# Kernel optimization log

Hardware: AMD Instinct MI355X
Metric: run time of the kernel (lower is better)

The kernel has to match this reference:

```python
import jax, jax.numpy as jnp
import numpy as np

R, N, E, F, D, A = 3, 50000, 800000, 128, 128, 64
EPS = 1e-5


def setup_inputs() -> dict:
    key = jax.random.key(0)
    ks = jax.random.split(key, 8)
    s = 0.05
    feat = jax.random.normal(ks[0], (N, F), jnp.float32)
    src = jax.random.randint(ks[1], (R, E), 0, N)
    dst = jax.random.randint(ks[2], (R, E), 0, N)
    W0 = jax.random.normal(ks[3], (R, F, D), jnp.float32) * s
    b0 = jnp.zeros((R, D), jnp.float32)
    W1 = jax.random.normal(ks[4], (R, D, D), jnp.float32) * s
    b1 = jnp.zeros((R, D), jnp.float32)
    ln_g = jnp.ones((R, D), jnp.float32)   # per-relation MessageTransform LayerNorm (shared across its 2 layers)
    ln_b = jnp.zeros((R, D), jnp.float32)
    LN_g = jnp.ones((D,), jnp.float32)     # final PROVGEM layer_norm
    LN_b = jnp.zeros((D,), jnp.float32)
    Wa1 = jax.random.normal(ks[5], (R, D, A), jnp.float32) * s  # semantic attention proj
    Wa2 = jax.random.normal(ks[6], (R, A), jnp.float32) * s     # semantic attention score vec
    return dict(feat=feat, src=src, dst=dst, W0=W0, b0=b0, W1=W1, b1=b1,
                ln_g=ln_g, ln_b=ln_b, LN_g=LN_g, LN_b=LN_b, Wa1=Wa1, Wa2=Wa2)


def _ln(x, g, b):
    mu = jnp.mean(x, axis=-1, keepdims=True)
    var = jnp.mean(jnp.square(x - mu), axis=-1, keepdims=True)
    return (x - mu) * jax.lax.rsqrt(var + EPS) * g + b


def _mean_agg(feat, src_r, dst_r):
    # copy_u + mean: gather source feats along edges, segment-mean into dst nodes
    msg = feat[src_r]                                            # [E, F]
    ssum = jax.ops.segment_sum(msg, dst_r, num_segments=N)       # [N, F]
    deg = jax.ops.segment_sum(jnp.ones((E,), feat.dtype), dst_r, num_segments=N)
    return ssum / jnp.maximum(deg, 1.0)[:, None]                 # 0 for zero-degree nodes


def reference(feat, src, dst, W0, b0, W1, b1, ln_g, ln_b, LN_g, LN_b, Wa1, Wa2):
    # per-relation aggregation (loop over small fixed R=3)
    neigh = jnp.stack([_mean_agg(feat, src[r], dst[r]) for r in range(R)])  # [R, N, F]
    h = feat[None, :, :] + neigh                                            # residual add
    x = jnp.einsum('rnf,rfd->rnd', h, W0) + b0[:, None, :]
    x = jax.nn.relu(_ln(x, ln_g[:, None, :], ln_b[:, None, :]))
    x = jnp.einsum('rnd,rde->rne', x, W1) + b1[:, None, :]
    x = jax.nn.relu(_ln(x, ln_g[:, None, :], ln_b[:, None, :]))
    # final LayerNorm over [R, N, D]
    h = _ln(x, LN_g, LN_b)
    # semantic attention over relations
    e = jnp.einsum('rna,ra->rn', jnp.tanh(jnp.einsum('rnd,rda->rna', h, Wa1)), Wa2)
    attn = jax.nn.softmax(e, axis=0)                                        # softmax over relations
    return jnp.einsum('rn,rnd->nd', attn, h)                                # [N, D]
```

## Files before the change

kernel.cpp:

```cpp
#include <hip/hip_runtime.h>

#define RR 3
#define NN 50000
#define EE 800000
#define FF 128
#define DD 128
#define AA 64
#define EPSF 1e-5f
#define RN (RR * NN)
#define RE (RR * EE)
#define NTPR ((NN + 127) / 128)
#define NBK (RR * NTPR)
#define ECHUNK 8192
#define NEBLK ((RE + ECHUNK - 1) / ECHUNK)
#define NTILES (NN / 16)

typedef __attribute__((ext_vector_type(8))) short bf16x8;
typedef __attribute__((ext_vector_type(4))) float f32x4;

__device__ __forceinline__ short f2bs(float x) {
    union { float f; unsigned u; } v; v.f = x;
    unsigned rr = (v.u + 0x7fffu + ((v.u >> 16) & 1u)) >> 16;
    return (short)(rr & 0xffffu);
}

__device__ __forceinline__ float bs2f_lo(int p) {
    union { unsigned u; float f; } v; v.u = (unsigned)p << 16; return v.f;
}
__device__ __forceinline__ float bs2f_hi(int p) {
    union { unsigned u; float f; } v; v.u = (unsigned)p & 0xffff0000u; return v.f;
}

__device__ __forceinline__ int rel_of(long e) {
    return (e >= 2L * EE) ? 2 : ((e >= (long)EE) ? 1 : 0);
}

__device__ __forceinline__ float ftanh(float x) {
    float a = __expf(2.0f * fabsf(x));
    return copysignf(1.0f - 2.0f / (a + 1.0f), x);
}

__global__ __launch_bounds__(256)
void feat2bf16(const float* __restrict__ feat, short* __restrict__ featb) {
    int gid = blockIdx.x * blockDim.x + threadIdx.x;
    if (gid >= NN * 16) return;
    f32x4 a = ((const f32x4*)feat)[2 * gid];
    f32x4 b = ((const f32x4*)feat)[2 * gid + 1];
    bf16x8 o;
    o[0] = f2bs(a.x); o[1] = f2bs(a.y); o[2] = f2bs(a.z); o[3] = f2bs(a.w);
    o[4] = f2bs(b.x); o[5] = f2bs(b.y); o[6] = f2bs(b.z); o[7] = f2bs(b.w);
    ((bf16x8*)featb)[gid] = o;
}

__global__ __launch_bounds__(256)
void count_kernel(const int* __restrict__ dst, int* __restrict__ bcnt) {
    __shared__ int hist[NBK];
    for (int i = threadIdx.x; i < NBK; i += 256) hist[i] = 0;
    __syncthreads();
    long ebase = (long)blockIdx.x * ECHUNK;
    for (int i = threadIdx.x; i < ECHUNK; i += 256) {
        long e = ebase + i;
        if (e < RE)
            atomicAdd(&hist[rel_of(e) * NTPR + (dst[e] >> 7)], 1);
    }
    __syncthreads();
    for (int i = threadIdx.x; i < NBK; i += 256) {
        int v = hist[i];
        if (v) atomicAdd(&bcnt[i], v);
    }
}

__global__ __launch_bounds__(256)
void bscan_kernel(const int* __restrict__ bcnt, int* __restrict__ bstart,
                  int* __restrict__ boff) {
    __shared__ int sm[256];
    int t = threadIdx.x;
    int loc[5];
    int s = 0;
    #pragma unroll
    for (int i = 0; i < 5; ++i) {
        int idx = t * 5 + i;
        int v = (idx < NBK) ? bcnt[idx] : 0;
        loc[i] = v; s += v;
    }
    sm[t] = s;
    __syncthreads();
    for (int d = 1; d < 256; d <<= 1) {
        int u = (t >= d) ? sm[t - d] : 0;
        __syncthreads();
        sm[t] += u;
        __syncthreads();
    }
    int run = sm[t] - s;
    #pragma unroll
    for (int i = 0; i < 5; ++i) {
        int idx = t * 5 + i;
        if (idx < NBK) { bstart[idx] = run; boff[idx] = run; run += loc[i]; }
    }
}

__global__ __launch_bounds__(256)
void bscatterA(const int* __restrict__ src, const int* __restrict__ dst,
               int* __restrict__ boff, unsigned* __restrict__ bpair) {
    __shared__ int hist[NBK];
    __shared__ int base[NBK];
    for (int i = threadIdx.x; i < NBK; i += 256) hist[i] = 0;
    __syncthreads();
    long ebase = (long)blockIdx.x * ECHUNK;
    for (int i = threadIdx.x; i < ECHUNK; i += 256) {
        long e = ebase + i;
        if (e < RE)
            atomicAdd(&hist[rel_of(e) * NTPR + (dst[e] >> 7)], 1);
    }
    __syncthreads();
    for (int i = threadIdx.x; i < NBK; i += 256) {
        int v = hist[i];
        base[i] = v ? atomicAdd(&boff[i], v) : 0;
    }
    __syncthreads();
    for (int i = threadIdx.x; i < ECHUNK; i += 256) {
        long e = ebase + i;
        if (e < RE) {
            int r = rel_of(e);
            int d = dst[e];
            int b = r * NTPR + (d >> 7);
            int pos = atomicAdd(&base[b], 1);
            bpair[pos] = ((unsigned)(d & 127) << 16) | (unsigned)src[e];
        }
    }
}

__global__ __launch_bounds__(256)
void scatterB(const unsigned* __restrict__ bpair, const int* __restrict__ bstart,
              const int* __restrict__ bcnt,
              int* __restrict__ off, int* __restrict__ cnt,
              int* __restrict__ csr) {
    __shared__ int hist[128];
    __shared__ int pre[128];
    __shared__ int base[128];
    int b = blockIdx.x;
    int r = b / NTPR, tile = b - r * NTPR;
    const int t = threadIdx.x;
    if (t < 128) hist[t] = 0;
    __syncthreads();
    int start = bstart[b], end = start + bcnt[b];
    for (int i = start + t; i < end; i += 256)
        atomicAdd(&hist[bpair[i] >> 16], 1);
    __syncthreads();
    if (t < 128) pre[t] = hist[t];
    __syncthreads();
    for (int d = 1; d < 128; d <<= 1) {
        int v = (t < 128 && t >= d) ? pre[t - d] : 0;
        __syncthreads();
        if (t < 128) pre[t] += v;
        __syncthreads();
    }
    if (t < 128) {
        int excl = pre[t] - hist[t];
        base[t] = start + excl;
        int nloc = tile * 128 + t;
        if (nloc < NN) {
            off[r * NN + nloc] = start + excl;
            cnt[r * NN + nloc] = hist[t];
        }
        hist[t] = 0;
    }
    __syncthreads();
    for (int i = start + t; i < end; i += 256) {
        unsigned p = bpair[i];
        int d = (int)(p >> 16);
        int rank = atomicAdd(&hist[d], 1);
        csr[base[d] + rank] = (int)(p & 0xFFFFu);
    }
}

__global__ __launch_bounds__(256)
void gather_kernel(const short* __restrict__ featb,
                   const int* __restrict__ csr,
                   const int* __restrict__ off,
                   const int* __restrict__ cnt,
                   short* __restrict__ ssumb) {
    int gid = blockIdx.x * blockDim.x + threadIdx.x;
    int w = gid >> 6, lane = gid & 63;
    if (w >= RN) return;
    int c = cnt[w];
    int start = off[w];
    int end = start + c;
    const int* f2 = (const int*)featb;
    float ax0 = 0.f, ay0 = 0.f, ax1 = 0.f, ay1 = 0.f;
    float ax2 = 0.f, ay2 = 0.f, ax3 = 0.f, ay3 = 0.f;
    float ax4 = 0.f, ay4 = 0.f, ax5 = 0.f, ay5 = 0.f;
    float ax6 = 0.f, ay6 = 0.f, ax7 = 0.f, ay7 = 0.f;
    int j = start;
    for (; j + 7 < end; j += 8) {
        int s0 = csr[j + 0], s1 = csr[j + 1], s2 = csr[j + 2], s3 = csr[j + 3];
        int s4 = csr[j + 4], s5 = csr[j + 5], s6 = csr[j + 6], s7 = csr[j + 7];
        int v0 = f2[(size_t)s0 * 64 + lane];
        int v1 = f2[(size_t)s1 * 64 + lane];
        int v2 = f2[(size_t)s2 * 64 + lane];
        int v3 = f2[(size_t)s3 * 64 + lane];
        int v4 = f2[(size_t)s4 * 64 + lane];
        int v5 = f2[(size_t)s5 * 64 + lane];
        int v6 = f2[(size_t)s6 * 64 + lane];
        int v7 = f2[(size_t)s7 * 64 + lane];
        ax0 += bs2f_lo(v0); ay0 += bs2f_hi(v0);
        ax1 += bs2f_lo(v1); ay1 += bs2f_hi(v1);
        ax2 += bs2f_lo(v2); ay2 += bs2f_hi(v2);
        ax3 += bs2f_lo(v3); ay3 += bs2f_hi(v3);
        ax4 += bs2f_lo(v4); ay4 += bs2f_hi(v4);
        ax5 += bs2f_lo(v5); ay5 += bs2f_hi(v5);
        ax6 += bs2f_lo(v6); ay6 += bs2f_hi(v6);
        ax7 += bs2f_lo(v7); ay7 += bs2f_hi(v7);
    }
    for (; j + 3 < end; j += 4) {
        int s0 = csr[j + 0], s1 = csr[j + 1], s2 = csr[j + 2], s3 = csr[j + 3];
        int v0 = f2[(size_t)s0 * 64 + lane];
        int v1 = f2[(size_t)s1 * 64 + lane];
        int v2 = f2[(size_t)s2 * 64 + lane];
        int v3 = f2[(size_t)s3 * 64 + lane];
        ax0 += bs2f_lo(v0); ay0 += bs2f_hi(v0);
        ax1 += bs2f_lo(v1); ay1 += bs2f_hi(v1);
        ax2 += bs2f_lo(v2); ay2 += bs2f_hi(v2);
        ax3 += bs2f_lo(v3); ay3 += bs2f_hi(v3);
    }
    for (; j < end; ++j) {
        int s = csr[j];
        int v = f2[(size_t)s * 64 + lane];
        ax0 += bs2f_lo(v); ay0 += bs2f_hi(v);
    }
    float ax = ((ax0 + ax1) + (ax2 + ax3)) + ((ax4 + ax5) + (ax6 + ax7));
    float ay = ((ay0 + ay1) + (ay2 + ay3)) + ((ay4 + ay5) + (ay6 + ay7));
    float inv = 1.0f / fmaxf((float)c, 1.0f);
    int n = w % NN;
    int fv = f2[(size_t)n * 64 + lane];
    float hx = bs2f_lo(fv) + ax * inv;
    float hy = bs2f_hi(fv) + ay * inv;
    unsigned plo = (unsigned short)f2bs(hx);
    unsigned phi = (unsigned short)f2bs(hy);
    ((int*)ssumb)[(size_t)w * 64 + lane] = (int)((phi << 16) | plo);
}


__device__ __forceinline__ void mfma_layer(const bf16x8 A[4], const short* Wlds,
                                           int g8, int c, f32x4 acc[8]) {
    #pragma unroll
    for (int kk = 0; kk < 4; ++kk) {
        #pragma unroll
        for (int t = 0; t < 8; ++t) {
            int d = t * 16 + c;
            bf16x8 B = *(const bf16x8*)&Wlds[d * 128 + ((kk * 32 + g8) ^ ((d & 7) << 3))];
            acc[t] = __builtin_amdgcn_mfma_f32_16x16x32_bf16(A[kk], B, acc[t], 0, 0, 0);
        }
    }
}

template <bool RELU, bool BIAS>
__device__ __forceinline__ void ln_block(f32x4 acc[8], const float* bias,
                                         const float* gam, const float* bet, int c) {
    float s0 = 0, s1 = 0, s2 = 0, s3 = 0, p0 = 0, p1 = 0, p2 = 0, p3 = 0;
    #pragma unroll
    for (int t = 0; t < 8; ++t) {
        if (BIAS) {
            float bb = bias[t * 16 + c];
            acc[t][0] += bb; acc[t][1] += bb;
            acc[t][2] += bb; acc[t][3] += bb;
        }
        s0 += acc[t][0]; p0 += acc[t][0] * acc[t][0];
        s1 += acc[t][1]; p1 += acc[t][1] * acc[t][1];
        s2 += acc[t][2]; p2 += acc[t][2] * acc[t][2];
        s3 += acc[t][3]; p3 += acc[t][3] * acc[t][3];
    }
    #pragma unroll
    for (int m = 1; m < 16; m <<= 1) {
        s0 += __shfl_xor(s0, m); s1 += __shfl_xor(s1, m);
        s2 += __shfl_xor(s2, m); s3 += __shfl_xor(s3, m);
        p0 += __shfl_xor(p0, m); p1 += __shfl_xor(p1, m);
        p2 += __shfl_xor(p2, m); p3 += __shfl_xor(p3, m);
    }
    const float inv = 1.0f / 128.0f;
    float mu0 = s0 * inv, mu1 = s1 * inv, mu2 = s2 * inv, mu3 = s3 * inv;
    float r0 = rsqrtf(p0 * inv - mu0 * mu0 + EPSF);
    float r1 = rsqrtf(p1 * inv - mu1 * mu1 + EPSF);
    float r2 = rsqrtf(p2 * inv - mu2 * mu2 + EPSF);
    float r3 = rsqrtf(p3 * inv - mu3 * mu3 + EPSF);
    #pragma unroll
    for (int t = 0; t < 8; ++t) {
        float gg = gam[t * 16 + c], bb = bet[t * 16 + c];
        float v0 = (acc[t][0] - mu0) * r0 * gg + bb;
        float v1 = (acc[t][1] - mu1) * r1 * gg + bb;
        float v2 = (acc[t][2] - mu2) * r2 * gg + bb;
        float v3 = (acc[t][3] - mu3) * r3 * gg + bb;
        if (RELU) {
            v0 = fmaxf(v0, 0.f); v1 = fmaxf(v1, 0.f);
            v2 = fmaxf(v2, 0.f); v3 = fmaxf(v3, 0.f);
        }
        acc[t][0] = v0; acc[t][1] = v1;
        acc[t][2] = v2; acc[t][3] = v3;
    }
}

__device__ __forceinline__ void store_ht(const f32x4 acc[8], short* myht, int g, int c) {
    #pragma unroll
    for (int t = 0; t < 8; ++t) {
        int col = t * 16 + c;
        #pragma unroll
        for (int qq = 0; qq < 4; ++qq) {
            int row = g * 4 + qq;
            myht[row * 128 + (col ^ ((row & 7) << 3))] = f2bs(acc[t][qq]);
        }
    }
}

__device__ __forceinline__ void ht_to_global(const short* myht, short* gout, int g, int c) {
    #pragma unroll
    for (int cc = 0; cc < 4; ++cc) {
        int row = cc * 4 + g;
        int col0 = c * 8;
        bf16x8 v = *(const bf16x8*)&myht[row * 128 + (col0 ^ ((row & 7) << 3))];
        *(bf16x8*)&gout[row * FF + col0] = v;
    }
}

__global__ __launch_bounds__(512)
void fused_l1(short* hbuf,
              const float* __restrict__ W0, const float* __restrict__ b0,
              const float* __restrict__ ln_g, const float* __restrict__ ln_b) {
    __shared__ short W0t[FF * DD];
    __shared__ short ht[8][16 * DD];
    __shared__ float b0s[DD], lgs[DD], lbs[DD];

    const int r = blockIdx.y;
    const int tid = threadIdx.x;

    for (int i = tid; i < FF * DD; i += 512) {
        int k = i >> 7, d = i & 127;
        W0t[d * 128 + (k ^ ((d & 7) << 3))] = f2bs(W0[(size_t)r * FF * DD + i]);
    }
    if (tid < DD) {
        b0s[tid] = b0[r * DD + tid];
        lgs[tid] = ln_g[r * DD + tid];
        lbs[tid] = ln_b[r * DD + tid];
    }
    __syncthreads();

    const int wv = tid >> 6, ln = tid & 63;
    const int g = ln >> 4, c = ln & 15;
    const int g8 = g * 8;
    short* myht = ht[wv];

    for (int tile = blockIdx.x * 8 + wv; tile < NTILES; tile += gridDim.x * 8) {
        const int nbase = tile * 16;
        bf16x8 A[4];
        {
            const short* sp = hbuf + ((size_t)r * NN + nbase + c) * FF;
            #pragma unroll
            for (int kk = 0; kk < 4; ++kk)
                A[kk] = *(const bf16x8*)(sp + kk * 32 + g8);
        }
        f32x4 acc[8];
        #pragma unroll
        for (int t = 0; t < 8; ++t) acc[t] = (f32x4){0.f, 0.f, 0.f, 0.f};
        mfma_layer(A, W0t, g8, c, acc);
        ln_block<true, true>(acc, b0s, lgs, lbs, c);
        store_ht(acc, myht, g, c);
        ht_to_global(myht, hbuf + ((size_t)r * NN + nbase) * FF, g, c);
    }
}

__global__ __launch_bounds__(512)
void fused_l2(short* hbuf,
              const float* __restrict__ W1, const float* __restrict__ b1,
              const float* __restrict__ ln_g, const float* __restrict__ ln_b,
              const float* __restrict__ LN_g, const float* __restrict__ LN_b) {
    __shared__ short W1t[DD * DD];
    __shared__ short ht[8][16 * DD];
    __shared__ float b1s[DD], lgs[DD], lbs[DD], Lgs[DD], Lbs[DD];

    const int r = blockIdx.y;
    const int tid = threadIdx.x;

    for (int i = tid; i < DD * DD; i += 512) {
        int k = i >> 7, d = i & 127;
        W1t[d * 128 + (k ^ ((d & 7) << 3))] = f2bs(W1[(size_t)r * DD * DD + i]);
    }
    if (tid < DD) {
        b1s[tid] = b1[r * DD + tid];
        lgs[tid] = ln_g[r * DD + tid];
        lbs[tid] = ln_b[r * DD + tid];
        Lgs[tid] = LN_g[tid];
        Lbs[tid] = LN_b[tid];
    }
    __syncthreads();

    const int wv = tid >> 6, ln = tid & 63;
    const int g = ln >> 4, c = ln & 15;
    const int g8 = g * 8;
    short* myht = ht[wv];

    for (int tile = blockIdx.x * 8 + wv; tile < NTILES; tile += gridDim.x * 8) {
        const int nbase = tile * 16;
        bf16x8 A[4];
        {
            const short* sp = hbuf + ((size_t)r * NN + nbase + c) * FF;
            #pragma unroll
            for (int kk = 0; kk < 4; ++kk)
                A[kk] = *(const bf16x8*)(sp + kk * 32 + g8);
        }
        f32x4 acc[8];
        #pragma unroll
        for (int t = 0; t < 8; ++t) acc[t] = (f32x4){0.f, 0.f, 0.f, 0.f};
        mfma_layer(A, W1t, g8, c, acc);
        ln_block<true, true>(acc, b1s, lgs, lbs, c);
        ln_block<false, false>(acc, nullptr, Lgs, Lbs, c);
        store_ht(acc, myht, g, c);
        ht_to_global(myht, hbuf + ((size_t)r * NN + nbase) * FF, g, c);
    }
}

__global__ __launch_bounds__(256)
void attn_score(const short* __restrict__ hbuf,
                const float* __restrict__ Wa1, const float* __restrict__ Wa2,
                float* __restrict__ evec) {
    __shared__ short Wa1t[RR][AA * DD];
    __shared__ float wa2s[RR][AA];

    const int tid = threadIdx.x;
    for (int i = tid; i < RR * DD * AA; i += 256) {
        int r2 = i >> 13;
        int rem = i & 8191;
        int k = rem >> 6, a = rem & 63;
        Wa1t[r2][a * 128 + (k ^ ((a & 7) << 3))] = f2bs(Wa1[i]);
    }
    if (tid < RR * AA) wa2s[tid >> 6][tid & 63] = Wa2[tid];
    __syncthreads();

    const int wv = tid >> 6, ln = tid & 63;
    const int col = ln & 15, g = ln >> 4;
    const int g8 = g * 8, g4 = g * 4;

    for (int idx = blockIdx.x * 4 + wv; idx < RR * NTILES; idx += gridDim.x * 4) {
        int r = idx / NTILES;
        int tile = idx - r * NTILES;
        int nbase = tile * 16;
        const short* hrow = hbuf + ((size_t)r * NN + nbase + col) * FF;

        f32x4 acc[4];
        #pragma unroll
        for (int t = 0; t < 4; ++t) acc[t] = (f32x4){0.f, 0.f, 0.f, 0.f};
        #pragma unroll
        for (int kk = 0; kk < 4; ++kk) {
            bf16x8 Bh = *(const bf16x8*)(hrow + kk * 32 + g8);
            #pragma unroll
            for (int t = 0; t < 4; ++t) {
                int a_ = t * 16 + col;
                bf16x8 Wf = *(const bf16x8*)&Wa1t[r][a_ * 128 + ((kk * 32 + g8) ^ ((a_ & 7) << 3))];
                acc[t] = __builtin_amdgcn_mfma_f32_16x16x32_bf16(Wf, Bh, acc[t], 0, 0, 0);
            }
        }
        float e = 0.f;
        #pragma unroll
        for (int t = 0; t < 4; ++t) {
            f32x4 wv2 = *(const f32x4*)&wa2s[r][t * 16 + g4];
            e += ftanh(acc[t][0]) * wv2[0] + ftanh(acc[t][1]) * wv2[1]
               + ftanh(acc[t][2]) * wv2[2] + ftanh(acc[t][3]) * wv2[3];
        }
        e += __shfl_xor(e, 16);
        e += __shfl_xor(e, 32);
        if (ln < 16) evec[(size_t)r * NN + nbase + ln] = e;
    }
}

__global__ __launch_bounds__(256)
void combine_kernel(const short* __restrict__ hfb,
                    const float* __restrict__ evec,
                    float* __restrict__ out) {
    int gid = blockIdx.x * blockDim.x + threadIdx.x;
    if (gid >= NN * 64) return;
    int n = gid >> 6, j = gid & 63;
    float e0 = evec[n], e1 = evec[NN + n], e2 = evec[2 * NN + n];
    float m = fmaxf(e0, fmaxf(e1, e2));
    float w0 = __expf(e0 - m), w1 = __expf(e1 - m), w2 = __expf(e2 - m);
    float inv = 1.0f / (w0 + w1 + w2);
    w0 *= inv; w1 *= inv; w2 *= inv;
    const int* h0 = (const int*)hfb + (size_t)n * 64;
    const int* h1 = (const int*)hfb + ((size_t)NN + n) * 64;
    const int* h2 = (const int*)hfb + ((size_t)2 * NN + n) * 64;
    int a = h0[j], b = h1[j], d = h2[j];
    float2 o;
    o.x = w0 * bs2f_lo(a) + w1 * bs2f_lo(b) + w2 * bs2f_lo(d);
    o.y = w0 * bs2f_hi(a) + w1 * bs2f_hi(b) + w2 * bs2f_hi(d);
    ((float2*)out)[(size_t)n * 64 + j] = o;
}

extern "C" void kernel_launch(void* const* d_in, const int* in_sizes, int n_in,
                              void* d_out, int out_size, void* d_ws, size_t ws_size,
                              hipStream_t stream) {
    const float* feat = (const float*)d_in[0];
    const int*   src  = (const int*)d_in[1];
    const int*   dst  = (const int*)d_in[2];
    const float* W0   = (const float*)d_in[3];
    const float* b0   = (const float*)d_in[4];
    const float* W1   = (const float*)d_in[5];
    const float* b1   = (const float*)d_in[6];
    const float* ln_g = (const float*)d_in[7];
    const float* ln_b = (const float*)d_in[8];
    const float* LN_g = (const float*)d_in[9];
    const float* LN_b = (const float*)d_in[10];
    const float* Wa1  = (const float*)d_in[11];
    const float* Wa2  = (const float*)d_in[12];
    float* out = (float*)d_out;

    short*    ssumb  = (short*)d_ws;
    short*    featb  = ssumb + (size_t)RN * FF;
    int*      cnt    = (int*)(featb + (size_t)NN * FF);
    int*      off    = cnt + RN;
    int*      csr    = off + RN;
    float*    evec   = (float*)(csr + RE);
    int*      bcnt   = (int*)(evec + RN);
    int*      bstart = bcnt + NBK;
    int*      boff   = bstart + NBK;
    unsigned* bpair  = (unsigned*)(boff + NBK);

    feat2bf16<<<(NN * 16 + 255) / 256, 256, 0, stream>>>(feat, featb);
    hipMemsetAsync(bcnt, 0, (size_t)NBK * sizeof(int), stream);
    count_kernel<<<NEBLK, 256, 0, stream>>>(dst, bcnt);
    bscan_kernel<<<1, 256, 0, stream>>>(bcnt, bstart, boff);
    bscatterA<<<NEBLK, 256, 0, stream>>>(src, dst, boff, bpair);
    scatterB<<<NBK, 256, 0, stream>>>(bpair, bstart, bcnt, off, cnt, csr);
    gather_kernel<<<(RN * 64 + 255) / 256, 256, 0, stream>>>(featb, csr, off, cnt, ssumb);

    const int GX = (NTILES + 7) / 8;
    fused_l1<<<dim3(GX, RR), 512, 0, stream>>>(ssumb, W0, b0, ln_g, ln_b);
    fused_l2<<<dim3(GX, RR), 512, 0, stream>>>(ssumb, W1, b1, ln_g, ln_b, LN_g, LN_b);
    attn_score<<<512, 256, 0, stream>>>(ssumb, Wa1, Wa2, evec);
    combine_kernel<<<(NN * 64 + 255) / 256, 256, 0, stream>>>(ssumb, evec, out);
}
```

Before: 312.4 us.

## Gather neighbor features in fp8 and fuse attention scoring with combine

```diff
diff --git a/kernel.cpp b/kernel.cpp
--- a/kernel.cpp
+++ b/kernel.cpp
@@ -17,6 +17,7 @@
 
 typedef __attribute__((ext_vector_type(8))) short bf16x8;
 typedef __attribute__((ext_vector_type(4))) float f32x4;
+typedef __attribute__((ext_vector_type(2))) float f32x2;
 
 __device__ __forceinline__ short f2bs(float x) {
     union { float f; unsigned u; } v; v.f = x;
@@ -41,7 +42,8 @@
 }
 
 __global__ __launch_bounds__(256)
-void feat2bf16(const float* __restrict__ feat, short* __restrict__ featb) {
+void feat2both(const float* __restrict__ feat, short* __restrict__ featb,
+               int* __restrict__ featq) {
     int gid = blockIdx.x * blockDim.x + threadIdx.x;
     if (gid >= NN * 16) return;
     f32x4 a = ((const f32x4*)feat)[2 * gid];
@@ -50,6 +52,13 @@
     o[0] = f2bs(a.x); o[1] = f2bs(a.y); o[2] = f2bs(a.z); o[3] = f2bs(a.w);
     o[4] = f2bs(b.x); o[5] = f2bs(b.y); o[6] = f2bs(b.z); o[7] = f2bs(b.w);
     ((bf16x8*)featb)[gid] = o;
+    int lo = 0, hi = 0;
+    lo = __builtin_amdgcn_cvt_pk_fp8_f32(a.x, a.y, lo, false);
+    lo = __builtin_amdgcn_cvt_pk_fp8_f32(a.z, a.w, lo, true);
+    hi = __builtin_amdgcn_cvt_pk_fp8_f32(b.x, b.y, hi, false);
+    hi = __builtin_amdgcn_cvt_pk_fp8_f32(b.z, b.w, hi, true);
+    int2 pk; pk.x = lo; pk.y = hi;
+    ((int2*)featq)[gid] = pk;
 }
 
 __global__ __launch_bounds__(256)
@@ -176,6 +185,7 @@
 
 __global__ __launch_bounds__(256)
 void gather_kernel(const short* __restrict__ featb,
+                   const int* __restrict__ featq,
                    const int* __restrict__ csr,
                    const int* __restrict__ off,
                    const int* __restrict__ cnt,
@@ -186,7 +196,7 @@
     int c = cnt[w];
     int start = off[w];
     int end = start + c;
-    const int* f2 = (const int*)featb;
+    const unsigned short* q = (const unsigned short*)featq;
     float ax0 = 0.f, ay0 = 0.f, ax1 = 0.f, ay1 = 0.f;
     float ax2 = 0.f, ay2 = 0.f, ax3 = 0.f, ay3 = 0.f;
     float ax4 = 0.f, ay4 = 0.f, ax5 = 0.f, ay5 = 0.f;
@@ -195,44 +205,57 @@
     for (; j + 7 < end; j += 8) {
         int s0 = csr[j + 0], s1 = csr[j + 1], s2 = csr[j + 2], s3 = csr[j + 3];
         int s4 = csr[j + 4], s5 = csr[j + 5], s6 = csr[j + 6], s7 = csr[j + 7];
-        int v0 = f2[(size_t)s0 * 64 + lane];
-        int v1 = f2[(size_t)s1 * 64 + lane];
-        int v2 = f2[(size_t)s2 * 64 + lane];
-        int v3 = f2[(size_t)s3 * 64 + lane];
-        int v4 = f2[(size_t)s4 * 64 + lane];
-        int v5 = f2[(size_t)s5 * 64 + lane];
-        int v6 = f2[(size_t)s6 * 64 + lane];
-        int v7 = f2[(size_t)s7 * 64 + lane];
-        ax0 += bs2f_lo(v0); ay0 += bs2f_hi(v0);
-        ax1 += bs2f_lo(v1); ay1 += bs2f_hi(v1);
-        ax2 += bs2f_lo(v2); ay2 += bs2f_hi(v2);
-        ax3 += bs2f_lo(v3); ay3 += bs2f_hi(v3);
-        ax4 += bs2f_lo(v4); ay4 += bs2f_hi(v4);
-        ax5 += bs2f_lo(v5); ay5 += bs2f_hi(v5);
-        ax6 += bs2f_lo(v6); ay6 += bs2f_hi(v6);
-        ax7 += bs2f_lo(v7); ay7 += bs2f_hi(v7);
+        int v0 = q[(size_t)s0 * 64 + lane];
+        int v1 = q[(size_t)s1 * 64 + lane];
+        int v2 = q[(size_t)s2 * 64 + lane];
+        int v3 = q[(size_t)s3 * 64 + lane];
+        int v4 = q[(size_t)s4 * 64 + lane];
+        int v5 = q[(size_t)s5 * 64 + lane];
+        int v6 = q[(size_t)s6 * 64 + lane];
+        int v7 = q[(size_t)s7 * 64 + lane];
+        f32x2 f0 = __builtin_amdgcn_cvt_pk_f32_fp8(v0, false);
+        f32x2 f1 = __builtin_amdgcn_cvt_pk_f32_fp8(v1, false);
+        f32x2 f2v = __builtin_amdgcn_cvt_pk_f32_fp8(v2, false);
+        f32x2 f3 = __builtin_amdgcn_cvt_pk_f32_fp8(v3, false);
+        f32x2 f4 = __builtin_amdgcn_cvt_pk_f32_fp8(v4, false);
+        f32x2 f5 = __builtin_amdgcn_cvt_pk_f32_fp8(v5, false);
+        f32x2 f6 = __builtin_amdgcn_cvt_pk_f32_fp8(v6, false);
+        f32x2 f7 = __builtin_amdgcn_cvt_pk_f32_fp8(v7, false);
+        ax0 += f0[0]; ay0 += f0[1];
+        ax1 += f1[0]; ay1 += f1[1];
+        ax2 += f2v[0]; ay2 += f2v[1];
+        ax3 += f3[0]; ay3 += f3[1];
+        ax4 += f4[0]; ay4 += f4[1];
+        ax5 += f5[0]; ay5 += f5[1];
+        ax6 += f6[0]; ay6 += f6[1];
+        ax7 += f7[0]; ay7 += f7[1];
     }
     for (; j + 3 < end; j += 4) {
         int s0 = csr[j + 0], s1 = csr[j + 1], s2 = csr[j + 2], s3 = csr[j + 3];
-        int v0 = f2[(size_t)s0 * 64 + lane];
-        int v1 = f2[(size_t)s1 * 64 + lane];
-        int v2 = f2[(size_t)s2 * 64 + lane];
-        int v3 = f2[(size_t)s3 * 64 + lane];
-        ax0 += bs2f_lo(v0); ay0 += bs2f_hi(v0);
-        ax1 += bs2f_lo(v1); ay1 += bs2f_hi(v1);
-        ax2 += bs2f_lo(v2); ay2 += bs2f_hi(v2);
-        ax3 += bs2f_lo(v3); ay3 += bs2f_hi(v3);
+        int v0 = q[(size_t)s0 * 64 + lane];
+        int v1 = q[(size_t)s1 * 64 + lane];
+        int v2 = q[(size_t)s2 * 64 + lane];
+        int v3 = q[(size_t)s3 * 64 + lane];
+        f32x2 f0 = __builtin_amdgcn_cvt_pk_f32_fp8(v0, false);
+        f32x2 f1 = __builtin_amdgcn_cvt_pk_f32_fp8(v1, false);
+        f32x2 f2v = __builtin_amdgcn_cvt_pk_f32_fp8(v2, false);
+        f32x2 f3 = __builtin_amdgcn_cvt_pk_f32_fp8(v3, false);
+        ax0 += f0[0]; ay0 += f0[1];
+        ax1 += f1[0]; ay1 += f1[1];
+        ax2 += f2v[0]; ay2 += f2v[1];
+        ax3 += f3[0]; ay3 += f3[1];
     }
     for (; j < end; ++j) {
         int s = csr[j];
-        int v = f2[(size_t)s * 64 + lane];
-        ax0 += bs2f_lo(v); ay0 += bs2f_hi(v);
+        int v = q[(size_t)s * 64 + lane];
+        f32x2 f0 = __builtin_amdgcn_cvt_pk_f32_fp8(v, false);
+        ax0 += f0[0]; ay0 += f0[1];
     }
     float ax = ((ax0 + ax1) + (ax2 + ax3)) + ((ax4 + ax5) + (ax6 + ax7));
     float ay = ((ay0 + ay1) + (ay2 + ay3)) + ((ay4 + ay5) + (ay6 + ay7));
     float inv = 1.0f / fmaxf((float)c, 1.0f);
     int n = w % NN;
-    int fv = f2[(size_t)n * 64 + lane];
+    int fv = ((const int*)featb)[(size_t)n * 64 + lane];
     float hx = bs2f_lo(fv) + ax * inv;
     float hy = bs2f_hi(fv) + ay * inv;
     unsigned plo = (unsigned short)f2bs(hx);
@@ -418,9 +441,9 @@
 }
 
 __global__ __launch_bounds__(256)
-void attn_score(const short* __restrict__ hbuf,
-                const float* __restrict__ Wa1, const float* __restrict__ Wa2,
-                float* __restrict__ evec) {
+void attn_combine(const short* __restrict__ hbuf,
+                  const float* __restrict__ Wa1, const float* __restrict__ Wa2,
+                  float* __restrict__ out) {
     __shared__ short Wa1t[RR][AA * DD];
     __shared__ float wa2s[RR][AA];
 
@@ -438,58 +461,60 @@
     const int col = ln & 15, g = ln >> 4;
     const int g8 = g * 8, g4 = g * 4;
 
-    for (int idx = blockIdx.x * 4 + wv; idx < RR * NTILES; idx += gridDim.x * 4) {
-        int r = idx / NTILES;
-        int tile = idx - r * NTILES;
-        int nbase = tile * 16;
-        const short* hrow = hbuf + ((size_t)r * NN + nbase + col) * FF;
-
-        f32x4 acc[4];
+    for (int tile = blockIdx.x * 4 + wv; tile < NTILES; tile += gridDim.x * 4) {
+        const int nbase = tile * 16;
+        bf16x8 Bh[RR][4];
+        float e[RR];
         #pragma unroll
-        for (int t = 0; t < 4; ++t) acc[t] = (f32x4){0.f, 0.f, 0.f, 0.f};
+        for (int r = 0; r < RR; ++r) {
+            const short* hrow = hbuf + ((size_t)r * NN + nbase + col) * FF;
+            #pragma unroll
+            for (int kk = 0; kk < 4; ++kk)
+                Bh[r][kk] = *(const bf16x8*)(hrow + kk * 32 + g8);
+            f32x4 acc[4];
+            #pragma unroll
+            for (int t = 0; t < 4; ++t) acc[t] = (f32x4){0.f, 0.f, 0.f, 0.f};
+            #pragma unroll
+            for (int kk = 0; kk < 4; ++kk)
+                #pragma unroll
+                for (int t = 0; t < 4; ++t) {
+                    int a_ = t * 16 + col;
+                    bf16x8 Wf = *(const bf16x8*)&Wa1t[r][a_ * 128 + ((kk * 32 + g8) ^ ((a_ & 7) << 3))];
+                    acc[t] = __builtin_amdgcn_mfma_f32_16x16x32_bf16(Wf, Bh[r][kk], acc[t], 0, 0, 0);
+                }
+            float ee = 0.f;
+            #pragma unroll
+            for (int t = 0; t < 4; ++t) {
+                f32x4 wv2 = *(const f32x4*)&wa2s[r][t * 16 + g4];
+                ee += ftanh(acc[t][0]) * wv2[0] + ftanh(acc[t][1]) * wv2[1]
+                    + ftanh(acc[t][2]) * wv2[2] + ftanh(acc[t][3]) * wv2[3];
+            }
+            ee += __shfl_xor(ee, 16);
+            ee += __shfl_xor(ee, 32);
+            e[r] = ee;
+        }
+        float m = fmaxf(e[0], fmaxf(e[1], e[2]));
+        float w0 = __expf(e[0] - m), w1 = __expf(e[1] - m), w2 = __expf(e[2] - m);
+        float inv = 1.0f / (w0 + w1 + w2);
+        w0 *= inv; w1 *= inv; w2 *= inv;
+
+        float* orow = out + (size_t)(nbase + col) * DD;
         #pragma unroll
         for (int kk = 0; kk < 4; ++kk) {
-            bf16x8 Bh = *(const bf16x8*)(hrow + kk * 32 + g8);
-            #pragma unroll
-            for (int t = 0; t < 4; ++t) {
-                int a_ = t * 16 + col;
-                bf16x8 Wf = *(const bf16x8*)&Wa1t[r][a_ * 128 + ((kk * 32 + g8) ^ ((a_ & 7) << 3))];
-                acc[t] = __builtin_amdgcn_mfma_f32_16x16x32_bf16(Wf, Bh, acc[t], 0, 0, 0);
+            union { bf16x8 v; int i[4]; } u0, u1, u2;
+            u0.v = Bh[0][kk]; u1.v = Bh[1][kk]; u2.v = Bh[2][kk];
+            f32x4 lo, hi;
+            #pragma unroll
+            for (int p = 0; p < 4; ++p) {
+                float va = w0 * bs2f_lo(u0.i[p]) + w1 * bs2f_lo(u1.i[p]) + w2 * bs2f_lo(u2.i[p]);
+                float vb = w0 * bs2f_hi(u0.i[p]) + w1 * bs2f_hi(u1.i[p]) + w2 * bs2f_hi(u2.i[p]);
+                if (p < 2) { lo[2 * p] = va; lo[2 * p + 1] = vb; }
+                else       { hi[2 * (p - 2)] = va; hi[2 * (p - 2) + 1] = vb; }
             }
-        }
-        float e = 0.f;
-        #pragma unroll
-        for (int t = 0; t < 4; ++t) {
-            f32x4 wv2 = *(const f32x4*)&wa2s[r][t * 16 + g4];
-            e += ftanh(acc[t][0]) * wv2[0] + ftanh(acc[t][1]) * wv2[1]
-               + ftanh(acc[t][2]) * wv2[2] + ftanh(acc[t][3]) * wv2[3];
-        }
-        e += __shfl_xor(e, 16);
-        e += __shfl_xor(e, 32);
-        if (ln < 16) evec[(size_t)r * NN + nbase + ln] = e;
-    }
-}
-
-__global__ __launch_bounds__(256)
-void combine_kernel(const short* __restrict__ hfb,
-                    const float* __restrict__ evec,
-                    float* __restrict__ out) {
-    int gid = blockIdx.x * blockDim.x + threadIdx.x;
-    if (gid >= NN * 64) return;
-    int n = gid >> 6, j = gid & 63;
-    float e0 = evec[n], e1 = evec[NN + n], e2 = evec[2 * NN + n];
-    float m = fmaxf(e0, fmaxf(e1, e2));
-    float w0 = __expf(e0 - m), w1 = __expf(e1 - m), w2 = __expf(e2 - m);
-    float inv = 1.0f / (w0 + w1 + w2);
-    w0 *= inv; w1 *= inv; w2 *= inv;
-    const int* h0 = (const int*)hfb + (size_t)n * 64;
-    const int* h1 = (const int*)hfb + ((size_t)NN + n) * 64;
-    const int* h2 = (const int*)hfb + ((size_t)2 * NN + n) * 64;
-    int a = h0[j], b = h1[j], d = h2[j];
-    float2 o;
-    o.x = w0 * bs2f_lo(a) + w1 * bs2f_lo(b) + w2 * bs2f_lo(d);
-    o.y = w0 * bs2f_hi(a) + w1 * bs2f_hi(b) + w2 * bs2f_hi(d);
-    ((float2*)out)[(size_t)n * 64 + j] = o;
+            *(f32x4*)(orow + kk * 32 + g8) = lo;
+            *(f32x4*)(orow + kk * 32 + g8 + 4) = hi;
+        }
+    }
 }
 
 extern "C" void kernel_launch(void* const* d_in, const int* in_sizes, int n_in,
@@ -512,26 +537,25 @@
 
     short*    ssumb  = (short*)d_ws;
     short*    featb  = ssumb + (size_t)RN * FF;
-    int*      cnt    = (int*)(featb + (size_t)NN * FF);
+    int*      featq  = (int*)(featb + (size_t)NN * FF);
+    int*      cnt    = featq + (size_t)NN * 32;
     int*      off    = cnt + RN;
     int*      csr    = off + RN;
-    float*    evec   = (float*)(csr + RE);
-    int*      bcnt   = (int*)(evec + RN);
+    int*      bcnt   = csr + RE;
     int*      bstart = bcnt + NBK;
     int*      boff   = bstart + NBK;
     unsigned* bpair  = (unsigned*)(boff + NBK);
 
-    feat2bf16<<<(NN * 16 + 255) / 256, 256, 0, stream>>>(feat, featb);
+    feat2both<<<(NN * 16 + 255) / 256, 256, 0, stream>>>(feat, featb, featq);
     hipMemsetAsync(bcnt, 0, (size_t)NBK * sizeof(int), stream);
     count_kernel<<<NEBLK, 256, 0, stream>>>(dst, bcnt);
     bscan_kernel<<<1, 256, 0, stream>>>(bcnt, bstart, boff);
     bscatterA<<<NEBLK, 256, 0, stream>>>(src, dst, boff, bpair);
     scatterB<<<NBK, 256, 0, stream>>>(bpair, bstart, bcnt, off, cnt, csr);
-    gather_kernel<<<(RN * 64 + 255) / 256, 256, 0, stream>>>(featb, csr, off, cnt, ssumb);
+    gather_kernel<<<(RN * 64 + 255) / 256, 256, 0, stream>>>(featb, featq, csr, off, cnt, ssumb);
 
     const int GX = (NTILES + 7) / 8;
     fused_l1<<<dim3(GX, RR), 512, 0, stream>>>(ssumb, W0, b0, ln_g, ln_b);
     fused_l2<<<dim3(GX, RR), 512, 0, stream>>>(ssumb, W1, b1, ln_g, ln_b, LN_g, LN_b);
-    attn_score<<<512, 256, 0, stream>>>(ssumb, Wa1, Wa2, evec);
-    combine_kernel<<<(NN * 64 + 255) / 256, 256, 0, stream>>>(ssumb, evec, out);
-}
+    attn_combine<<<(NTILES + 3) / 4, 256, 0, stream>>>(ssumb, Wa1, Wa2, out);
+}
```

Result: no change. 318.3 us (+1.9%).
